# Kernel optimization log

Measured on AMD Instinct MI355X. Metric: run time of the kernel, lower is better.

Reference implementation:

```python
import jax, jax.numpy as jnp
import numpy as np

N_NODES = 50000
N_EDGES = 1600000
IN_DIM = 128
OUT_DIM = 32
N_HEADS = 4
NEG_SLOPE = 0.01  # default F.leaky_relu slope


def setup_inputs() -> dict:
    key = jax.random.key(0)
    k1, k2, k3, k4, k5 = jax.random.split(key, 5)
    h = jax.random.normal(k1, (N_NODES, IN_DIM), dtype=jnp.float32)
    # per-head fc weight [H, out, in] and attn weight [H, 2*out]
    W = jax.random.normal(k2, (N_HEADS, OUT_DIM, IN_DIM), dtype=jnp.float32) * (1.0 / np.sqrt(IN_DIM))
    a = jax.random.normal(k3, (N_HEADS, 2 * OUT_DIM), dtype=jnp.float32) * (1.0 / np.sqrt(2 * OUT_DIM))
    src = jax.random.randint(k4, (N_EDGES,), 0, N_NODES, dtype=jnp.int64)
    dst = jax.random.randint(k5, (N_EDGES,), 0, N_NODES, dtype=jnp.int64)
    return {"h": h, "W": W, "a": a, "src": src, "dst": dst}


def reference(h, W, a, src, dst):
    N = h.shape[0]
    O = W.shape[1]
    # per-head linear projection: [N, H, O]
    z = jnp.einsum('ni,hoi->nho', h, W)
    zs = z[src]  # [E, H, O] gathered source features
    zd = z[dst]  # [E, H, O] gathered destination features
    # attention logits: a . concat(zs, zd) per head -> [E, H]
    e = jnp.einsum('eho,ho->eh', zs, a[:, :O]) + jnp.einsum('eho,ho->eh', zd, a[:, O:])
    e = jnp.where(e >= 0, e, NEG_SLOPE * e)  # leaky_relu
    # edge softmax over incoming edges of each dst node (per head)
    e_max = jax.ops.segment_max(e, dst, num_segments=N)          # [N, H]
    e_max = jnp.where(jnp.isfinite(e_max), e_max, 0.0)
    ex = jnp.exp(e - e_max[dst])                                  # [E, H]
    denom = jax.ops.segment_sum(ex, dst, num_segments=N)         # [N, H]
    alpha = ex / jnp.where(denom[dst] > 0, denom[dst], 1.0)      # [E, H]
    # weighted scatter-sum of source features -> [N, H, O]
    out = jax.ops.segment_sum(alpha[:, :, None] * zs, dst, num_segments=N)
    # concat heads -> [N, H*O]
    return out.reshape(N, -1)
```

## Files before the change

kernel.cpp:

```cpp
#include <hip/hip_runtime.h>
#include <hip/hip_bf16.h>
#include <stdint.h>


#define NN 50000
#define NE 1600000
#define IN_DIM 128
#define OC 128
#define NBSH 6
#define NBUCK ((NN + 63) >> 6)
#define CAP 2560
#define CURS 16
#define BIN_BLOCKS 256
#define EPB ((NE + BIN_BLOCKS - 1) / BIN_BLOCKS)

__device__ __forceinline__ float lrelu(float x) { return x >= 0.f ? x : 0.01f * x; }

__global__ __launch_bounds__(256) void k_gemm_s(const float* __restrict__ h,
                                                const float* __restrict__ W,
                                                const float* __restrict__ a,
                                                __hip_bfloat16* __restrict__ zb,
                                                float* __restrict__ ssrc,
                                                float* __restrict__ sdst) {
    __shared__ float hs[64][65];
    __shared__ float ws[64][129];
    const int t  = threadIdx.x;
    const int n0 = blockIdx.x * 64;
    const int tx = t & 31;
    const int ty = t >> 5;

    float acc[8][4];
#pragma unroll
    for (int i = 0; i < 8; ++i)
#pragma unroll
        for (int j = 0; j < 4; ++j) acc[i][j] = 0.f;

    for (int kt = 0; kt < IN_DIM; kt += 64) {
#pragma unroll
        for (int s = 0; s < 4; ++s) {
            const int idx4 = t + s * 256;
            const int n    = idx4 >> 4;
            const int kk   = (idx4 & 15) << 2;
            const int gn   = n0 + n;
            float4 v = make_float4(0.f, 0.f, 0.f, 0.f);
            if (gn < NN) v = *(const float4*)(h + (size_t)gn * IN_DIM + kt + kk);
            hs[kk + 0][n] = v.x; hs[kk + 1][n] = v.y;
            hs[kk + 2][n] = v.z; hs[kk + 3][n] = v.w;
        }
#pragma unroll
        for (int s = 0; s < 8; ++s) {
            const int idx4 = t + s * 256;
            const int c    = idx4 >> 4;
            const int kk   = (idx4 & 15) << 2;
            const float4 v = *(const float4*)(W + (size_t)c * IN_DIM + kt + kk);
            ws[kk + 0][c] = v.x; ws[kk + 1][c] = v.y;
            ws[kk + 2][c] = v.z; ws[kk + 3][c] = v.w;
        }
        __syncthreads();
#pragma unroll 4
        for (int k = 0; k < 64; ++k) {
            float wv[4], hv[8];
#pragma unroll
            for (int j = 0; j < 4; ++j) wv[j] = ws[k][tx + 32 * j];
#pragma unroll
            for (int i = 0; i < 8; ++i) hv[i] = hs[k][ty + 8 * i];
#pragma unroll
            for (int i = 0; i < 8; ++i)
#pragma unroll
                for (int j = 0; j < 4; ++j) acc[i][j] = fmaf(hv[i], wv[j], acc[i][j]);
        }
        __syncthreads();
    }
#pragma unroll
    for (int i = 0; i < 8; ++i) {
        const int gn = n0 + ty + 8 * i;
        if (gn < NN) {
#pragma unroll
            for (int j = 0; j < 4; ++j)
                zb[(size_t)gn * OC + tx + 32 * j] = __float2bfloat16(acc[i][j]);
        }
    }
    float as[4], ad[4];
#pragma unroll
    for (int j = 0; j < 4; ++j) {
        as[j] = a[j * 64 + tx];
        ad[j] = a[j * 64 + 32 + tx];
    }
#pragma unroll
    for (int i = 0; i < 8; ++i) {
        const int gn = n0 + ty + 8 * i;
#pragma unroll
        for (int j = 0; j < 4; ++j) {
            float ps = acc[i][j] * as[j];
            float pd = acc[i][j] * ad[j];
#pragma unroll
            for (int off = 16; off > 0; off >>= 1) {
                ps += __shfl_xor(ps, off);
                pd += __shfl_xor(pd, off);
            }
            if (tx == 0 && gn < NN) {
                ssrc[gn * 4 + j] = ps;
                sdst[gn * 4 + j] = pd;
            }
        }
    }
}

__global__ __launch_bounds__(256) void k_init(int* __restrict__ cursor) {
    const int b = blockIdx.x * 256 + threadIdx.x;
    if (b < NBUCK) cursor[b * CURS] = b * CAP;
}

__global__ __launch_bounds__(256) void k_bin2(const int* __restrict__ src,
                                              const int* __restrict__ dst,
                                              int* __restrict__ cursor,
                                              uint32_t* __restrict__ ebuf) {
    __shared__ int hb[NBUCK];
    __shared__ int ofs[NBUCK];
    const int t    = threadIdx.x;
    const int ebeg = blockIdx.x * EPB;
    const int eend = min(ebeg + EPB, NE);
    for (int i = t; i < NBUCK; i += 256) hb[i] = 0;
    __syncthreads();
    for (int e = ebeg + t; e < eend; e += 256)
        atomicAdd(&hb[dst[e] >> NBSH], 1);
    __syncthreads();
    for (int i = t; i < NBUCK; i += 256) {
        const int c = hb[i];
        ofs[i] = (c > 0) ? atomicAdd(&cursor[i * CURS], c) : 0;
        hb[i] = 0;
    }
    __syncthreads();
    for (int e = ebeg + t; e < eend; e += 256) {
        const int d = dst[e];
        const int b = d >> NBSH;
        const int p = ofs[b] + atomicAdd(&hb[b], 1);
        if (p < (b + 1) * CAP)
            ebuf[p] = (uint32_t)src[e] | ((uint32_t)(d & 63) << 16);
    }
}

__global__ __launch_bounds__(512) void k_gatb(const uint32_t* __restrict__ zb,
                                              const float4* __restrict__ ssrc,
                                              const float4* __restrict__ sdst,
                                              const int* __restrict__ cursor,
                                              const uint32_t* __restrict__ ebuf,
                                              float* __restrict__ out) {
    __shared__ unsigned short elist[CAP];
    __shared__ float2 lp[8][64][4];
    __shared__ float4 sdl[64];
    __shared__ int cnt[64], cur[64], basel[64];
    const int b     = blockIdx.x;
    const int tid   = threadIdx.x;
    const int bbase = b * CAP;
    const int ecnt  = min(cursor[b * CURS], bbase + CAP) - bbase;

    if (tid < 64) cnt[tid] = 0;
    if (tid >= 64 && tid < 128) {
        const int gnode = (b << NBSH) + tid - 64;
        sdl[tid - 64] = (gnode < NN) ? sdst[gnode] : make_float4(0.f, 0.f, 0.f, 0.f);
    }
    __syncthreads();
    for (int i = tid; i < ecnt; i += 512)
        atomicAdd(&cnt[(ebuf[bbase + i] >> 16) & 63], 1);
    __syncthreads();
    if (tid < 64) {
        const int d = cnt[tid];
        int v = d;
#pragma unroll
        for (int off = 1; off < 64; off <<= 1) {
            const int u = __shfl_up(v, off);
            if (tid >= off) v += u;
        }
        basel[tid] = v - d;
        cur[tid]   = v - d;
    }
    __syncthreads();
    for (int i = tid; i < ecnt; i += 512) {
        const uint32_t v = ebuf[bbase + i];
        const int dl = (v >> 16) & 63;
        const int p  = atomicAdd(&cur[dl], 1);
        elist[p] = (unsigned short)(v & 0xffffu);
    }
    __syncthreads();

    const int wid    = tid >> 6;
    const int lane   = tid & 63;
    const int lane16 = lane & 15;
    const int grp    = lane >> 4;
    const int hsel   = lane16 >> 2;
#pragma unroll 1
    for (int nl = wid * 8; nl < wid * 8 + 8; ++nl) {
        const int gnode = (b << NBSH) + nl;
        if (gnode >= NN) break;
        const int d  = cnt[nl];
        const int s0 = basel[nl];
        const float4 sd = sdl[nl];

        float acc[8];
#pragma unroll
        for (int i = 0; i < 8; ++i) acc[i] = 0.f;
        float dn0 = 0.f, dn1 = 0.f, dn2 = 0.f, dn3 = 0.f;

        for (int base = 0; base < d; base += 64) {
            const int myj = base + lane;
            int sid_l = 0;
            float x0 = 0.f, x1 = 0.f, x2 = 0.f, x3 = 0.f;
            if (myj < d) {
                sid_l = elist[s0 + myj];
                const float4 ss = ssrc[sid_l];
                x0 = __expf(lrelu(ss.x + sd.x));
                x1 = __expf(lrelu(ss.y + sd.y));
                x2 = __expf(lrelu(ss.z + sd.z));
                x3 = __expf(lrelu(ss.w + sd.w));
                dn0 += x0; dn1 += x1; dn2 += x2; dn3 += x3;
            }
            const float sf = __builtin_bit_cast(float, sid_l);
            float4* lq = (float4*)&lp[wid][lane][0];
            lq[0] = make_float4(sf, x0, sf, x1);
            lq[1] = make_float4(sf, x2, sf, x3);

            const int cntc = min(64, d - base);
            const int nit  = (cntc + 3) >> 2;
#pragma unroll 2
            for (int it = 0; it < nit; ++it) {
                const int e4 = (it << 2) + grp;
                const float2 pw = lp[wid][e4][hsel];
                const int   sid = __builtin_bit_cast(int, pw.x);
                const float w   = pw.y;
                const uint4 Z = *(const uint4*)(zb + ((size_t)sid << 6) + (lane16 << 2));
                acc[0] = fmaf(w, __builtin_bit_cast(float, Z.x << 16),          acc[0]);
                acc[1] = fmaf(w, __builtin_bit_cast(float, Z.x & 0xffff0000u),  acc[1]);
                acc[2] = fmaf(w, __builtin_bit_cast(float, Z.y << 16),          acc[2]);
                acc[3] = fmaf(w, __builtin_bit_cast(float, Z.y & 0xffff0000u),  acc[3]);
                acc[4] = fmaf(w, __builtin_bit_cast(float, Z.z << 16),          acc[4]);
                acc[5] = fmaf(w, __builtin_bit_cast(float, Z.z & 0xffff0000u),  acc[5]);
                acc[6] = fmaf(w, __builtin_bit_cast(float, Z.w << 16),          acc[6]);
                acc[7] = fmaf(w, __builtin_bit_cast(float, Z.w & 0xffff0000u),  acc[7]);
            }
        }
#pragma unroll
        for (int i = 0; i < 8; ++i) {
            acc[i] += __shfl_xor(acc[i], 16);
            acc[i] += __shfl_xor(acc[i], 32);
        }
#pragma unroll
        for (int off = 32; off > 0; off >>= 1) {
            dn0 += __shfl_xor(dn0, off);
            dn1 += __shfl_xor(dn1, off);
            dn2 += __shfl_xor(dn2, off);
            dn3 += __shfl_xor(dn3, off);
        }
        const float dsel = (hsel == 0) ? dn0 : (hsel == 1) ? dn1 : (hsel == 2) ? dn2 : dn3;
        const float inv  = (dsel > 0.f) ? 1.0f / dsel : 0.f;
        if (grp == 0) {
            float* op = out + (size_t)gnode * OC + (lane16 << 3);
            *(float4*)(op)     = make_float4(acc[0]*inv, acc[1]*inv, acc[2]*inv, acc[3]*inv);
            *(float4*)(op + 4) = make_float4(acc[4]*inv, acc[5]*inv, acc[6]*inv, acc[7]*inv);
        }
    }
}

extern "C" void kernel_launch(void* const* d_in, const int* in_sizes, int n_in,
                              void* d_out, int out_size, void* d_ws, size_t ws_size,
                              hipStream_t stream) {
    const float* h_in = (const float*)d_in[0];
    const float* W    = (const float*)d_in[1];
    const float* a    = (const float*)d_in[2];
    const int*   src  = (const int*)d_in[3];
    const int*   dst  = (const int*)d_in[4];
    float*       out  = (float*)d_out;

    char* w = (char*)d_ws;
    __hip_bfloat16* zb = (__hip_bfloat16*)(w);
    float*    ssrc     = (float*)(w + 12800000);
    float*    sdst     = (float*)(w + 13600000);
    int*      cursor   = (int*)(w + 14400000);
    uint32_t* ebuf     = (uint32_t*)(w + 14450048);

    k_gemm_s<<<(NN + 63) / 64, 256, 0, stream>>>(h_in, W, a, zb, ssrc, sdst);
    k_init  <<<(NBUCK + 255) / 256, 256, 0, stream>>>(cursor);
    k_bin2  <<<BIN_BLOCKS, 256, 0, stream>>>(src, dst, cursor, ebuf);
    k_gatb  <<<NBUCK, 512, 0, stream>>>((const uint32_t*)zb,
                                        (const float4*)ssrc, (const float4*)sdst,
                                        cursor, ebuf, out);
}
```

Baseline: 235.8 us.

## Retile projection GEMM to 128-node blocks with 8x8 register tiles, drop init kernel

The projection GEMM now processes 128 nodes per block with each thread holding an 8x8 accumulator tile. Shared-memory reads are float4-vectorized, the bf16 stores are packed into 16-byte writes, and the attention dot products are reduced with fewer shuffles. The cursor-init kernel is replaced by a hipMemsetAsync, and bucket offsets become relative to each bucket's base. Together these aim to raise arithmetic intensity in the GEMM and remove one kernel launch, at the cost of more registers per thread and lower occupancy.

```diff
diff --git a/kernel.cpp b/kernel.cpp
--- a/kernel.cpp
+++ b/kernel.cpp
@@ -22,93 +22,85 @@
                                                 __hip_bfloat16* __restrict__ zb,
                                                 float* __restrict__ ssrc,
                                                 float* __restrict__ sdst) {
-    __shared__ float hs[64][65];
-    __shared__ float ws[64][129];
+    __shared__ float hs[32][132];
+    __shared__ float ws[32][132];
     const int t  = threadIdx.x;
-    const int n0 = blockIdx.x * 64;
-    const int tx = t & 31;
-    const int ty = t >> 5;
-
-    float acc[8][4];
+    const int n0 = blockIdx.x * 128;
+    const int u  = t & 15;
+    const int v  = t >> 4;
+
+    float acc[8][8];
 #pragma unroll
     for (int i = 0; i < 8; ++i)
 #pragma unroll
-        for (int j = 0; j < 4; ++j) acc[i][j] = 0.f;
-
-    for (int kt = 0; kt < IN_DIM; kt += 64) {
+        for (int j = 0; j < 8; ++j) acc[i][j] = 0.f;
+
+    for (int kt = 0; kt < IN_DIM; kt += 32) {
 #pragma unroll
         for (int s = 0; s < 4; ++s) {
-            const int idx4 = t + s * 256;
-            const int n    = idx4 >> 4;
-            const int kk   = (idx4 & 15) << 2;
-            const int gn   = n0 + n;
-            float4 v = make_float4(0.f, 0.f, 0.f, 0.f);
-            if (gn < NN) v = *(const float4*)(h + (size_t)gn * IN_DIM + kt + kk);
-            hs[kk + 0][n] = v.x; hs[kk + 1][n] = v.y;
-            hs[kk + 2][n] = v.z; hs[kk + 3][n] = v.w;
-        }
-#pragma unroll
-        for (int s = 0; s < 8; ++s) {
-            const int idx4 = t + s * 256;
-            const int c    = idx4 >> 4;
-            const int kk   = (idx4 & 15) << 2;
-            const float4 v = *(const float4*)(W + (size_t)c * IN_DIM + kt + kk);
-            ws[kk + 0][c] = v.x; ws[kk + 1][c] = v.y;
-            ws[kk + 2][c] = v.z; ws[kk + 3][c] = v.w;
+            const int idx = t + s * 256;
+            const int r   = idx >> 3;
+            const int kk  = (idx & 7) << 2;
+            const int gn  = n0 + r;
+            float4 hv = make_float4(0.f, 0.f, 0.f, 0.f);
+            if (gn < NN) hv = *(const float4*)(h + (size_t)gn * IN_DIM + kt + kk);
+            hs[kk + 0][r] = hv.x; hs[kk + 1][r] = hv.y;
+            hs[kk + 2][r] = hv.z; hs[kk + 3][r] = hv.w;
+            const float4 wv = *(const float4*)(W + (size_t)r * IN_DIM + kt + kk);
+            ws[kk + 0][r] = wv.x; ws[kk + 1][r] = wv.y;
+            ws[kk + 2][r] = wv.z; ws[kk + 3][r] = wv.w;
         }
         __syncthreads();
 #pragma unroll 4
-        for (int k = 0; k < 64; ++k) {
-            float wv[4], hv[8];
-#pragma unroll
-            for (int j = 0; j < 4; ++j) wv[j] = ws[k][tx + 32 * j];
-#pragma unroll
-            for (int i = 0; i < 8; ++i) hv[i] = hs[k][ty + 8 * i];
+        for (int k = 0; k < 32; ++k) {
+            const float4 h0 = *(const float4*)&hs[k][8 * u];
+            const float4 h1 = *(const float4*)&hs[k][8 * u + 4];
+            const float4 w0 = *(const float4*)&ws[k][8 * v];
+            const float4 w1 = *(const float4*)&ws[k][8 * v + 4];
+            const float hv[8] = {h0.x, h0.y, h0.z, h0.w, h1.x, h1.y, h1.z, h1.w};
+            const float wv[8] = {w0.x, w0.y, w0.z, w0.w, w1.x, w1.y, w1.z, w1.w};
 #pragma unroll
             for (int i = 0; i < 8; ++i)
 #pragma unroll
-                for (int j = 0; j < 4; ++j) acc[i][j] = fmaf(hv[i], wv[j], acc[i][j]);
+                for (int j = 0; j < 8; ++j) acc[i][j] = fmaf(hv[i], wv[j], acc[i][j]);
         }
         __syncthreads();
     }
+
 #pragma unroll
     for (int i = 0; i < 8; ++i) {
-        const int gn = n0 + ty + 8 * i;
+        const int gn = n0 + 8 * u + i;
         if (gn < NN) {
-#pragma unroll
-            for (int j = 0; j < 4; ++j)
-                zb[(size_t)gn * OC + tx + 32 * j] = __float2bfloat16(acc[i][j]);
-        }
-    }
-    float as[4], ad[4];
-#pragma unroll
-    for (int j = 0; j < 4; ++j) {
-        as[j] = a[j * 64 + tx];
-        ad[j] = a[j * 64 + 32 + tx];
+            __hip_bfloat16 bv[8];
+#pragma unroll
+            for (int j = 0; j < 8; ++j) bv[j] = __float2bfloat16(acc[i][j]);
+            *(uint4*)(zb + (size_t)gn * OC + 8 * v) = *(const uint4*)bv;
+        }
+    }
+
+    const int head = v >> 2;
+    float as[8], ad[8];
+#pragma unroll
+    for (int j = 0; j < 8; ++j) {
+        as[j] = a[head * 64 + 8 * (v & 3) + j];
+        ad[j] = a[head * 64 + 32 + 8 * (v & 3) + j];
     }
 #pragma unroll
     for (int i = 0; i < 8; ++i) {
-        const int gn = n0 + ty + 8 * i;
-#pragma unroll
-        for (int j = 0; j < 4; ++j) {
-            float ps = acc[i][j] * as[j];
-            float pd = acc[i][j] * ad[j];
-#pragma unroll
-            for (int off = 16; off > 0; off >>= 1) {
-                ps += __shfl_xor(ps, off);
-                pd += __shfl_xor(pd, off);
-            }
-            if (tx == 0 && gn < NN) {
-                ssrc[gn * 4 + j] = ps;
-                sdst[gn * 4 + j] = pd;
-            }
-        }
-    }
-}
-
-__global__ __launch_bounds__(256) void k_init(int* __restrict__ cursor) {
-    const int b = blockIdx.x * 256 + threadIdx.x;
-    if (b < NBUCK) cursor[b * CURS] = b * CAP;
+        float ps = 0.f, pd = 0.f;
+#pragma unroll
+        for (int j = 0; j < 8; ++j) {
+            ps = fmaf(acc[i][j], as[j], ps);
+            pd = fmaf(acc[i][j], ad[j], pd);
+        }
+        ps += __shfl_xor(ps, 16); ps += __shfl_xor(ps, 32);
+        pd += __shfl_xor(pd, 16); pd += __shfl_xor(pd, 32);
+        const int gn = n0 + 8 * u + i;
+        if ((v & 3) == 0 && gn < NN) {
+            ssrc[gn * 4 + head] = ps;
+            sdst[gn * 4 + head] = pd;
+        }
+    }
 }
 
 __global__ __launch_bounds__(256) void k_bin2(const int* __restrict__ src,
@@ -135,8 +127,8 @@
         const int d = dst[e];
         const int b = d >> NBSH;
         const int p = ofs[b] + atomicAdd(&hb[b], 1);
-        if (p < (b + 1) * CAP)
-            ebuf[p] = (uint32_t)src[e] | ((uint32_t)(d & 63) << 16);
+        if (p < CAP)
+            ebuf[b * CAP + p] = (uint32_t)src[e] | ((uint32_t)(d & 63) << 16);
     }
 }
 
@@ -153,7 +145,7 @@
     const int b     = blockIdx.x;
     const int tid   = threadIdx.x;
     const int bbase = b * CAP;
-    const int ecnt  = min(cursor[b * CURS], bbase + CAP) - bbase;
+    const int ecnt  = min(cursor[b * CURS], CAP);
 
     if (tid < 64) cnt[tid] = 0;
     if (tid >= 64 && tid < 128) {
@@ -169,8 +161,8 @@
         int v = d;
 #pragma unroll
         for (int off = 1; off < 64; off <<= 1) {
-            const int u = __shfl_up(v, off);
-            if (tid >= off) v += u;
+            const int uu = __shfl_up(v, off);
+            if (tid >= off) v += uu;
         }
         basel[tid] = v - d;
         cur[tid]   = v - d;
@@ -278,8 +270,9 @@
     int*      cursor   = (int*)(w + 14400000);
     uint32_t* ebuf     = (uint32_t*)(w + 14450048);
 
-    k_gemm_s<<<(NN + 63) / 64, 256, 0, stream>>>(h_in, W, a, zb, ssrc, sdst);
-    k_init  <<<(NBUCK + 255) / 256, 256, 0, stream>>>(cursor);
+    hipMemsetAsync(cursor, 0, NBUCK * CURS * 4, stream);
+
+    k_gemm_s<<<(NN + 127) / 128, 256, 0, stream>>>(h_in, W, a, zb, ssrc, sdst);
     k_bin2  <<<BIN_BLOCKS, 256, 0, stream>>>(src, dst, cursor, ebuf);
     k_gatb  <<<NBUCK, 512, 0, stream>>>((const uint32_t*)zb,
                                         (const float4*)ssrc, (const float4*)sdst,
```

After: 225.5 us. -4.4%, faster.
